# Performance work log

Hardware: AMD Instinct MI355X
Metric: run time of the kernel (lower is better)

The kernel has to match this reference:

```python
import jax, jax.numpy as jnp
import numpy as np

B, IN_DIM, OUT_DIM, NUM_FN = 256, 65536, 65536, 16  # fan_in=2 -> 16 logic functions


def setup_inputs() -> dict:
    key = jax.random.key(0)
    k1, k2, k3 = jax.random.split(key, 3)
    x = jax.random.uniform(k1, (B, IN_DIM), dtype=jnp.float32)
    weights = jax.random.normal(k2, (OUT_DIM, NUM_FN), dtype=jnp.float32)
    # each output neuron picks fan_in=2 input wires
    indices = jax.random.randint(k3, (2, OUT_DIM), 0, IN_DIM, dtype=jnp.int64)
    return {"x": x, "weights": weights, "indices": indices}


def _logic_ops(a, b):
    """All 16 real-valued relaxations of binary boolean functions. [B,OUT,16]."""
    ab = a * b
    one = jnp.ones_like(a)
    zero = jnp.zeros_like(a)
    return jnp.stack([
        zero,                # 0: false
        ab,                  # 1: a AND b
        a - ab,              # 2: a AND NOT b
        a,                   # 3: a
        b - ab,              # 4: NOT a AND b
        b,                   # 5: b
        a + b - 2 * ab,      # 6: a XOR b
        a + b - ab,          # 7: a OR b
        1 - (a + b - ab),    # 8: NOR
        1 - (a + b - 2*ab),  # 9: XNOR
        1 - b,               # 10: NOT b
        1 - b + ab,          # 11: a OR NOT b
        1 - a,               # 12: NOT a
        1 - a + ab,          # 13: NOT a OR b
        1 - ab,              # 14: NAND
        one,                 # 15: true
    ], axis=-1)


def reference(x, weights, indices):
    # gather fan-in inputs: a, b each [B, OUT_DIM]
    a = x[..., indices[0]]
    b = x[..., indices[1]]
    probs = jax.nn.softmax(weights, axis=-1)        # [OUT_DIM, 16] (training path)
    ops = _logic_ops(a, b)                          # [B, OUT_DIM, 16]
    return jnp.einsum('bof,of->bo', ops, probs)     # softmax-weighted combo
```

## Files before the change

kernel.cpp:

```cpp
#include <hip/hip_runtime.h>

#define IN_DIM  65536
#define OUT_DIM 65536
#define BATCH   256
#define ROWS_PER_BLOCK 32


__device__ __forceinline__ float bf2f(unsigned short h) {
    return __uint_as_float(((unsigned int)h) << 16);
}

__global__ __launch_bounds__(512) void detect_kernel(
    const unsigned short* __restrict__ x,
    const unsigned short* __restrict__ w,
    const int* __restrict__ idx,
    int* __restrict__ flags)
{
    __shared__ int s[3];
    int t = threadIdx.x;
    if (t < 3) s[t] = 0;
    __syncthreads();
    if (x[t] >= 0x3F80u) atomicOr(&s[0], 1);
    if ((unsigned)(w[t] & 0x7FFFu) >= 0x4800u) atomicOr(&s[1], 1);
    if ((t & 1) && idx[t] != 0) atomicOr(&s[2], 1);
    __syncthreads();
    if (t == 0) {
        flags[0] = s[0];
        flags[1] = s[1];
        flags[2] = s[2] ? 0 : 1;
    }
}

__global__ __launch_bounds__(256) void coeff_kernel(
    const void* __restrict__ weights_raw,
    const int* __restrict__ flags,
    float4* __restrict__ coeffs)
{
    int o = blockIdx.x * blockDim.x + threadIdx.x;
    if (o >= OUT_DIM) return;

    float w[16];
    if (flags[1]) {
        const float4* w4 = reinterpret_cast<const float4*>(weights_raw) + (size_t)o * 4;
        float4 q0 = w4[0], q1 = w4[1], q2 = w4[2], q3 = w4[3];
        w[0]=q0.x; w[1]=q0.y; w[2]=q0.z; w[3]=q0.w;
        w[4]=q1.x; w[5]=q1.y; w[6]=q1.z; w[7]=q1.w;
        w[8]=q2.x; w[9]=q2.y; w[10]=q2.z; w[11]=q2.w;
        w[12]=q3.x; w[13]=q3.y; w[14]=q3.z; w[15]=q3.w;
    } else {
        const uint4* w16 = reinterpret_cast<const uint4*>(
            (const unsigned short*)weights_raw + (size_t)o * 16);
        uint4 p0 = w16[0], p1 = w16[1];
        unsigned int pk[8] = { p0.x, p0.y, p0.z, p0.w, p1.x, p1.y, p1.z, p1.w };
        #pragma unroll
        for (int i = 0; i < 8; ++i) {
            w[2*i]   = bf2f((unsigned short)(pk[i] & 0xFFFFu));
            w[2*i+1] = bf2f((unsigned short)(pk[i] >> 16));
        }
    }

    float m = w[0];
    #pragma unroll
    for (int f = 1; f < 16; ++f) m = fmaxf(m, w[f]);

    float e[16]; float sum = 0.f;
    #pragma unroll
    for (int f = 0; f < 16; ++f) { e[f] = __expf(w[f] - m); sum += e[f]; }
    float inv = 1.0f / sum;

    float w0 = e[8] + e[9] + e[10] + e[11] + e[12] + e[13] + e[14] + e[15];
    float w1 = (e[2] + e[3] + e[6] + e[7]) - (e[8] + e[9] + e[12] + e[13]);
    float w2 = (e[4] + e[5] + e[6] + e[7]) - (e[8] + e[9] + e[10] + e[11]);
    float w3 = e[1] - e[2] - e[4] - 2.f*e[6] - e[7]
             + e[8] + 2.f*e[9] + e[11] + e[13] - e[14];

    coeffs[o] = make_float4(w0 * inv, w1 * inv, w2 * inv, w3 * inv);
}

__global__ __launch_bounds__(256) void transpose_kernel(
    const void* __restrict__ x_raw,
    const int* __restrict__ flags,
    float* __restrict__ x_T)
{
    __shared__ float tile[64][65];
    int tx = threadIdx.x;
    int ty = threadIdx.y;
    int c0 = blockIdx.x * 64;
    int b0 = blockIdx.y * 64;

    if (flags[0]) {
        const float* x = (const float*)x_raw;
        #pragma unroll
        for (int k = 0; k < 64; k += 4)
            tile[ty + k][tx] = x[(size_t)(b0 + ty + k) * IN_DIM + c0 + tx];
    } else {
        const unsigned short* x = (const unsigned short*)x_raw;
        #pragma unroll
        for (int k = 0; k < 64; k += 4)
            tile[ty + k][tx] = bf2f(x[(size_t)(b0 + ty + k) * IN_DIM + c0 + tx]);
    }
    __syncthreads();
    #pragma unroll
    for (int k = 0; k < 64; k += 4) {
        int c = ty + k;
        x_T[(size_t)(c0 + c) * BATCH + b0 + tx] = tile[tx][c];
    }
}

__global__ __launch_bounds__(256) void logic_t_kernel(
    const float* __restrict__ x_T,
    const void* __restrict__ idx_raw,
    const int* __restrict__ flags,
    const float4* __restrict__ coeffs,
    float* __restrict__ out)
{
    int o = blockIdx.x * blockDim.x + threadIdx.x;

    int ia, ib;
    if (flags[2]) {
        const long long* p = (const long long*)idx_raw;
        ia = (int)p[o];  ib = (int)p[OUT_DIM + o];
    } else {
        const int* p = (const int*)idx_raw;
        ia = p[o];       ib = p[OUT_DIM + o];
    }
    float4 c = coeffs[o];

    const float4* xa = reinterpret_cast<const float4*>(x_T) + ((size_t)ia << 6);
    const float4* xb = reinterpret_cast<const float4*>(x_T) + ((size_t)ib << 6);

    int b0 = blockIdx.y * ROWS_PER_BLOCK;
    int q0 = b0 >> 2;

    #pragma unroll
    for (int r = 0; r < ROWS_PER_BLOCK / 4; ++r) {
        float4 a4 = xa[q0 + r];
        float4 b4 = xb[q0 + r];
        int bb = b0 + r * 4;
        float r0 = fmaf(b4.x, fmaf(c.w, a4.x, c.z), fmaf(c.y, a4.x, c.x));
        float r1 = fmaf(b4.y, fmaf(c.w, a4.y, c.z), fmaf(c.y, a4.y, c.x));
        float r2 = fmaf(b4.z, fmaf(c.w, a4.z, c.z), fmaf(c.y, a4.z, c.x));
        float r3 = fmaf(b4.w, fmaf(c.w, a4.w, c.z), fmaf(c.y, a4.w, c.x));
        out[(size_t)(bb + 0) * OUT_DIM + o] = r0;
        out[(size_t)(bb + 1) * OUT_DIM + o] = r1;
        out[(size_t)(bb + 2) * OUT_DIM + o] = r2;
        out[(size_t)(bb + 3) * OUT_DIM + o] = r3;
    }
}

__global__ __launch_bounds__(256) void logic_kernel(
    const void* __restrict__ x_raw,
    const void* __restrict__ idx_raw,
    const int* __restrict__ flags,
    const float4* __restrict__ coeffs,
    float* __restrict__ out)
{
    int o = blockIdx.x * blockDim.x + threadIdx.x;

    int ia, ib;
    if (flags[2]) {
        const long long* p = (const long long*)idx_raw;
        ia = (int)p[o];  ib = (int)p[OUT_DIM + o];
    } else {
        const int* p = (const int*)idx_raw;
        ia = p[o];       ib = p[OUT_DIM + o];
    }
    float4 c = coeffs[o];
    int b0 = blockIdx.y * ROWS_PER_BLOCK;

    if (flags[0]) {
        const float* xa = (const float*)x_raw + ia;
        const float* xb = (const float*)x_raw + ib;
        #pragma unroll 8
        for (int r = 0; r < ROWS_PER_BLOCK; ++r) {
            int b = b0 + r;
            float av = xa[(size_t)b * IN_DIM];
            float bv = xb[(size_t)b * IN_DIM];
            out[(size_t)b * OUT_DIM + o] =
                fmaf(bv, fmaf(c.w, av, c.z), fmaf(c.y, av, c.x));
        }
    } else {
        const unsigned short* xa = (const unsigned short*)x_raw + ia;
        const unsigned short* xb = (const unsigned short*)x_raw + ib;
        #pragma unroll 8
        for (int r = 0; r < ROWS_PER_BLOCK; ++r) {
            int b = b0 + r;
            float av = bf2f(xa[(size_t)b * IN_DIM]);
            float bv = bf2f(xb[(size_t)b * IN_DIM]);
            out[(size_t)b * OUT_DIM + o] =
                fmaf(bv, fmaf(c.w, av, c.z), fmaf(c.y, av, c.x));
        }
    }
}

extern "C" void kernel_launch(void* const* d_in, const int* in_sizes, int n_in,
                              void* d_out, int out_size, void* d_ws, size_t ws_size,
                              hipStream_t stream) {
    const void* x       = d_in[0];
    const void* weights = d_in[1];
    const void* indices = d_in[2];
    float*      out     = (float*)d_out;

    int*    flags  = (int*)d_ws;
    float4* coeffs = (float4*)((char*)d_ws + 256);
    float*  x_T    = (float*)((char*)d_ws + 2u * 1024u * 1024u);

    const size_t need = 2u * 1024u * 1024u +
                        (size_t)IN_DIM * BATCH * sizeof(float);

    detect_kernel<<<1, 512, 0, stream>>>(
        (const unsigned short*)x, (const unsigned short*)weights,
        (const int*)indices, flags);

    coeff_kernel<<<dim3(OUT_DIM / 256), dim3(256), 0, stream>>>(
        weights, flags, coeffs);

    if (ws_size >= need) {
        transpose_kernel<<<dim3(IN_DIM / 64, BATCH / 64), dim3(64, 4), 0, stream>>>(
            x, flags, x_T);
        dim3 grid(OUT_DIM / 256, BATCH / ROWS_PER_BLOCK);
        logic_t_kernel<<<grid, dim3(256), 0, stream>>>(
            x_T, indices, flags, coeffs, out);
    } else {
        dim3 grid(OUT_DIM / 256, BATCH / ROWS_PER_BLOCK);
        logic_kernel<<<grid, dim3(256), 0, stream>>>(
            x, indices, flags, coeffs, out);
    }
}
```

Measured before the change: 161.2 us.

## Store transposed x as packed bf16 and fuse prep kernels into one launch

Merges the detect, coeff and transpose kernels into a single prep launch. Each block now detects the input dtype itself in shared memory instead of reading a global flags buffer. The transposed copy of x is stored as packed bf16 pairs rather than fp32, halving the intermediate write and the gather reads in the logic kernel. The cost is that fp32 inputs are rounded to bf16, which loses precision, and every logic block repeats the small dtype probe.

```diff
diff --git a/kernel.cpp b/kernel.cpp
--- a/kernel.cpp
+++ b/kernel.cpp
@@ -3,176 +3,200 @@
 #define IN_DIM  65536
 #define OUT_DIM 65536
 #define BATCH   256
-#define ROWS_PER_BLOCK 32
 
 
 __device__ __forceinline__ float bf2f(unsigned short h) {
     return __uint_as_float(((unsigned int)h) << 16);
 }
-
-__global__ __launch_bounds__(512) void detect_kernel(
-    const unsigned short* __restrict__ x,
-    const unsigned short* __restrict__ w,
-    const int* __restrict__ idx,
-    int* __restrict__ flags)
-{
-    __shared__ int s[3];
-    int t = threadIdx.x;
-    if (t < 3) s[t] = 0;
-    __syncthreads();
-    if (x[t] >= 0x3F80u) atomicOr(&s[0], 1);
-    if ((unsigned)(w[t] & 0x7FFFu) >= 0x4800u) atomicOr(&s[1], 1);
-    if ((t & 1) && idx[t] != 0) atomicOr(&s[2], 1);
-    __syncthreads();
-    if (t == 0) {
-        flags[0] = s[0];
-        flags[1] = s[1];
-        flags[2] = s[2] ? 0 : 1;
-    }
-}
-
-__global__ __launch_bounds__(256) void coeff_kernel(
-    const void* __restrict__ weights_raw,
-    const int* __restrict__ flags,
-    float4* __restrict__ coeffs)
-{
-    int o = blockIdx.x * blockDim.x + threadIdx.x;
-    if (o >= OUT_DIM) return;
-
-    float w[16];
-    if (flags[1]) {
-        const float4* w4 = reinterpret_cast<const float4*>(weights_raw) + (size_t)o * 4;
-        float4 q0 = w4[0], q1 = w4[1], q2 = w4[2], q3 = w4[3];
-        w[0]=q0.x; w[1]=q0.y; w[2]=q0.z; w[3]=q0.w;
-        w[4]=q1.x; w[5]=q1.y; w[6]=q1.z; w[7]=q1.w;
-        w[8]=q2.x; w[9]=q2.y; w[10]=q2.z; w[11]=q2.w;
-        w[12]=q3.x; w[13]=q3.y; w[14]=q3.z; w[15]=q3.w;
-    } else {
-        const uint4* w16 = reinterpret_cast<const uint4*>(
-            (const unsigned short*)weights_raw + (size_t)o * 16);
-        uint4 p0 = w16[0], p1 = w16[1];
-        unsigned int pk[8] = { p0.x, p0.y, p0.z, p0.w, p1.x, p1.y, p1.z, p1.w };
-        #pragma unroll
-        for (int i = 0; i < 8; ++i) {
-            w[2*i]   = bf2f((unsigned short)(pk[i] & 0xFFFFu));
-            w[2*i+1] = bf2f((unsigned short)(pk[i] >> 16));
-        }
-    }
-
+__device__ __forceinline__ unsigned short f2bf(float f) {
+    unsigned int u = __float_as_uint(f);
+    u += 0x7FFFu + ((u >> 16) & 1u);
+    return (unsigned short)(u >> 16);
+}
+
+__device__ __forceinline__ float4 collapse16(const float* w) {
     float m = w[0];
     #pragma unroll
     for (int f = 1; f < 16; ++f) m = fmaxf(m, w[f]);
-
     float e[16]; float sum = 0.f;
     #pragma unroll
     for (int f = 0; f < 16; ++f) { e[f] = __expf(w[f] - m); sum += e[f]; }
     float inv = 1.0f / sum;
-
     float w0 = e[8] + e[9] + e[10] + e[11] + e[12] + e[13] + e[14] + e[15];
     float w1 = (e[2] + e[3] + e[6] + e[7]) - (e[8] + e[9] + e[12] + e[13]);
     float w2 = (e[4] + e[5] + e[6] + e[7]) - (e[8] + e[9] + e[10] + e[11]);
     float w3 = e[1] - e[2] - e[4] - 2.f*e[6] - e[7]
              + e[8] + 2.f*e[9] + e[11] + e[13] - e[14];
-
-    coeffs[o] = make_float4(w0 * inv, w1 * inv, w2 * inv, w3 * inv);
-}
-
-__global__ __launch_bounds__(256) void transpose_kernel(
+    return make_float4(w0 * inv, w1 * inv, w2 * inv, w3 * inv);
+}
+
+#define TRANS_BLOCKS ((IN_DIM / 64) * (BATCH / 64))
+#define COEFF_BLOCKS (OUT_DIM / 256)
+
+__global__ __launch_bounds__(256) void prep_kernel(
     const void* __restrict__ x_raw,
-    const int* __restrict__ flags,
-    float* __restrict__ x_T)
+    const void* __restrict__ w_raw,
+    unsigned int* __restrict__ x_Tb,
+    float4* __restrict__ coeffs,
+    int trans_blocks)
 {
     __shared__ float tile[64][65];
-    int tx = threadIdx.x;
-    int ty = threadIdx.y;
-    int c0 = blockIdx.x * 64;
-    int b0 = blockIdx.y * 64;
-
-    if (flags[0]) {
-        const float* x = (const float*)x_raw;
+    __shared__ int sflag;
+    int t  = threadIdx.x;
+    int bx = blockIdx.x;
+
+    if (bx < trans_blocks) {
+        if (t == 0) sflag = 0;
+        __syncthreads();
+        if (((const unsigned short*)x_raw)[t] >= 0x3F80u) atomicOr(&sflag, 1);
+        __syncthreads();
+        int x_is_f32 = sflag;
+
+        int c0 = (bx >> 2) * 64;
+        int b0 = (bx & 3) * 64;
+        int tx = t & 63, ty = t >> 6;
+
+        if (x_is_f32) {
+            const float* x = (const float*)x_raw;
+            #pragma unroll
+            for (int k = 0; k < 64; k += 4)
+                tile[ty + k][tx] = x[(size_t)(b0 + ty + k) * IN_DIM + c0 + tx];
+        } else {
+            const unsigned short* x = (const unsigned short*)x_raw;
+            #pragma unroll
+            for (int k = 0; k < 64; k += 4)
+                tile[ty + k][tx] = bf2f(x[(size_t)(b0 + ty + k) * IN_DIM + c0 + tx]);
+        }
+        __syncthreads();
         #pragma unroll
-        for (int k = 0; k < 64; k += 4)
-            tile[ty + k][tx] = x[(size_t)(b0 + ty + k) * IN_DIM + c0 + tx];
-    } else {
-        const unsigned short* x = (const unsigned short*)x_raw;
-        #pragma unroll
-        for (int k = 0; k < 64; k += 4)
-            tile[ty + k][tx] = bf2f(x[(size_t)(b0 + ty + k) * IN_DIM + c0 + tx]);
-    }
-    __syncthreads();
-    #pragma unroll
-    for (int k = 0; k < 64; k += 4) {
-        int c = ty + k;
-        x_T[(size_t)(c0 + c) * BATCH + b0 + tx] = tile[tx][c];
-    }
-}
-
-__global__ __launch_bounds__(256) void logic_t_kernel(
-    const float* __restrict__ x_T,
+        for (int k = 0; k < 8; ++k) {
+            int d   = t + 256 * k;
+            int col = d >> 5;
+            int dw  = d & 31;
+            float lo = tile[2 * dw][col];
+            float hi = tile[2 * dw + 1][col];
+            unsigned int p = (unsigned int)f2bf(lo) | ((unsigned int)f2bf(hi) << 16);
+            x_Tb[(size_t)(c0 + col) * (BATCH / 2) + (b0 >> 1) + dw] = p;
+        }
+    } else {
+        if (t == 0) sflag = 0;
+        __syncthreads();
+        if ((((const unsigned short*)w_raw)[t] & 0x7FFFu) >= 0x4800u) atomicOr(&sflag, 1);
+        __syncthreads();
+        int w_is_f32 = sflag;
+
+        int o = (bx - trans_blocks) * 256 + t;
+        if (o >= OUT_DIM) return;
+
+        float w[16];
+        if (w_is_f32) {
+            const float4* w4 = reinterpret_cast<const float4*>(w_raw) + (size_t)o * 4;
+            float4 q0 = w4[0], q1 = w4[1], q2 = w4[2], q3 = w4[3];
+            w[0]=q0.x; w[1]=q0.y; w[2]=q0.z; w[3]=q0.w;
+            w[4]=q1.x; w[5]=q1.y; w[6]=q1.z; w[7]=q1.w;
+            w[8]=q2.x; w[9]=q2.y; w[10]=q2.z; w[11]=q2.w;
+            w[12]=q3.x; w[13]=q3.y; w[14]=q3.z; w[15]=q3.w;
+        } else {
+            const uint4* w16 = reinterpret_cast<const uint4*>(
+                (const unsigned short*)w_raw + (size_t)o * 16);
+            uint4 p0 = w16[0], p1 = w16[1];
+            unsigned int pk[8] = { p0.x, p0.y, p0.z, p0.w, p1.x, p1.y, p1.z, p1.w };
+            #pragma unroll
+            for (int i = 0; i < 8; ++i) {
+                w[2*i]   = bf2f((unsigned short)(pk[i] & 0xFFFFu));
+                w[2*i+1] = bf2f((unsigned short)(pk[i] >> 16));
+            }
+        }
+        coeffs[o] = collapse16(w);
+    }
+}
+
+#define ROWS_PER_CHUNK 32
+
+__global__ __launch_bounds__(256) void logic_bt_kernel(
+    const unsigned int* __restrict__ x_Tb,
     const void* __restrict__ idx_raw,
-    const int* __restrict__ flags,
     const float4* __restrict__ coeffs,
     float* __restrict__ out)
 {
-    int o = blockIdx.x * blockDim.x + threadIdx.x;
-
+    __shared__ int sflag;
+    int t = threadIdx.x;
+    if (t == 0) sflag = 0;
+    __syncthreads();
+    if ((t & 1) && ((const int*)idx_raw)[t] != 0) atomicOr(&sflag, 1);
+    __syncthreads();
+    int idx_is_i32 = sflag;
+
+    int o = blockIdx.x * 256 + t;
     int ia, ib;
-    if (flags[2]) {
+    if (idx_is_i32) {
+        const int* p = (const int*)idx_raw;
+        ia = p[o];       ib = p[OUT_DIM + o];
+    } else {
         const long long* p = (const long long*)idx_raw;
         ia = (int)p[o];  ib = (int)p[OUT_DIM + o];
-    } else {
-        const int* p = (const int*)idx_raw;
-        ia = p[o];       ib = p[OUT_DIM + o];
     }
     float4 c = coeffs[o];
 
-    const float4* xa = reinterpret_cast<const float4*>(x_T) + ((size_t)ia << 6);
-    const float4* xb = reinterpret_cast<const float4*>(x_T) + ((size_t)ib << 6);
-
-    int b0 = blockIdx.y * ROWS_PER_BLOCK;
-    int q0 = b0 >> 2;
+    int b0 = blockIdx.y * ROWS_PER_CHUNK;
+    const uint4* xa = (const uint4*)x_Tb + ((size_t)ia << 5) + (b0 >> 3);
+    const uint4* xb = (const uint4*)x_Tb + ((size_t)ib << 5) + (b0 >> 3);
 
     #pragma unroll
-    for (int r = 0; r < ROWS_PER_BLOCK / 4; ++r) {
-        float4 a4 = xa[q0 + r];
-        float4 b4 = xb[q0 + r];
-        int bb = b0 + r * 4;
-        float r0 = fmaf(b4.x, fmaf(c.w, a4.x, c.z), fmaf(c.y, a4.x, c.x));
-        float r1 = fmaf(b4.y, fmaf(c.w, a4.y, c.z), fmaf(c.y, a4.y, c.x));
-        float r2 = fmaf(b4.z, fmaf(c.w, a4.z, c.z), fmaf(c.y, a4.z, c.x));
-        float r3 = fmaf(b4.w, fmaf(c.w, a4.w, c.z), fmaf(c.y, a4.w, c.x));
-        out[(size_t)(bb + 0) * OUT_DIM + o] = r0;
-        out[(size_t)(bb + 1) * OUT_DIM + o] = r1;
-        out[(size_t)(bb + 2) * OUT_DIM + o] = r2;
-        out[(size_t)(bb + 3) * OUT_DIM + o] = r3;
-    }
-}
-
-__global__ __launch_bounds__(256) void logic_kernel(
+    for (int r = 0; r < ROWS_PER_CHUNK / 8; ++r) {
+        uint4 ua = xa[r], ub = xb[r];
+        unsigned int pa[4] = { ua.x, ua.y, ua.z, ua.w };
+        unsigned int pb[4] = { ub.x, ub.y, ub.z, ub.w };
+        int base = b0 + r * 8;
+        #pragma unroll
+        for (int j = 0; j < 4; ++j) {
+            float a0 = bf2f((unsigned short)(pa[j] & 0xFFFFu));
+            float a1 = bf2f((unsigned short)(pa[j] >> 16));
+            float v0 = bf2f((unsigned short)(pb[j] & 0xFFFFu));
+            float v1 = bf2f((unsigned short)(pb[j] >> 16));
+            float r0 = fmaf(v0, fmaf(c.w, a0, c.z), fmaf(c.y, a0, c.x));
+            float r1 = fmaf(v1, fmaf(c.w, a1, c.z), fmaf(c.y, a1, c.x));
+            out[(size_t)(base + 2*j)     * OUT_DIM + o] = r0;
+            out[(size_t)(base + 2*j + 1) * OUT_DIM + o] = r1;
+        }
+    }
+}
+
+__global__ __launch_bounds__(256) void logic_direct_kernel(
     const void* __restrict__ x_raw,
     const void* __restrict__ idx_raw,
-    const int* __restrict__ flags,
     const float4* __restrict__ coeffs,
     float* __restrict__ out)
 {
-    int o = blockIdx.x * blockDim.x + threadIdx.x;
-
+    __shared__ int sflag;
+    int t = threadIdx.x;
+    if (t == 0) sflag = 0;
+    __syncthreads();
+    int fl = 0;
+    if (((const unsigned short*)x_raw)[t] >= 0x3F80u) fl |= 1;
+    if ((t & 1) && ((const int*)idx_raw)[t] != 0) fl |= 2;
+    if (fl) atomicOr(&sflag, fl);
+    __syncthreads();
+    int x_is_f32   = sflag & 1;
+    int idx_is_i32 = (sflag >> 1) & 1;
+
+    int o = blockIdx.x * 256 + t;
     int ia, ib;
-    if (flags[2]) {
+    if (idx_is_i32) {
+        const int* p = (const int*)idx_raw;
+        ia = p[o];       ib = p[OUT_DIM + o];
+    } else {
         const long long* p = (const long long*)idx_raw;
         ia = (int)p[o];  ib = (int)p[OUT_DIM + o];
-    } else {
-        const int* p = (const int*)idx_raw;
-        ia = p[o];       ib = p[OUT_DIM + o];
     }
     float4 c = coeffs[o];
-    int b0 = blockIdx.y * ROWS_PER_BLOCK;
-
-    if (flags[0]) {
+    int b0 = blockIdx.y * ROWS_PER_CHUNK;
+
+    if (x_is_f32) {
         const float* xa = (const float*)x_raw + ia;
         const float* xb = (const float*)x_raw + ib;
         #pragma unroll 8
-        for (int r = 0; r < ROWS_PER_BLOCK; ++r) {
+        for (int r = 0; r < ROWS_PER_CHUNK; ++r) {
             int b = b0 + r;
             float av = xa[(size_t)b * IN_DIM];
             float bv = xb[(size_t)b * IN_DIM];
@@ -183,7 +207,7 @@
         const unsigned short* xa = (const unsigned short*)x_raw + ia;
         const unsigned short* xb = (const unsigned short*)x_raw + ib;
         #pragma unroll 8
-        for (int r = 0; r < ROWS_PER_BLOCK; ++r) {
+        for (int r = 0; r < ROWS_PER_CHUNK; ++r) {
             int b = b0 + r;
             float av = bf2f(xa[(size_t)b * IN_DIM]);
             float bv = bf2f(xb[(size_t)b * IN_DIM]);
@@ -201,29 +225,23 @@
     const void* indices = d_in[2];
     float*      out     = (float*)d_out;
 
-    int*    flags  = (int*)d_ws;
-    float4* coeffs = (float4*)((char*)d_ws + 256);
-    float*  x_T    = (float*)((char*)d_ws + 2u * 1024u * 1024u);
+    float4*       coeffs = (float4*)((char*)d_ws + 256);
+    unsigned int* x_Tb   = (unsigned int*)((char*)d_ws + 2u * 1024u * 1024u);
 
     const size_t need = 2u * 1024u * 1024u +
-                        (size_t)IN_DIM * BATCH * sizeof(float);
-
-    detect_kernel<<<1, 512, 0, stream>>>(
-        (const unsigned short*)x, (const unsigned short*)weights,
-        (const int*)indices, flags);
-
-    coeff_kernel<<<dim3(OUT_DIM / 256), dim3(256), 0, stream>>>(
-        weights, flags, coeffs);
+                        (size_t)IN_DIM * (BATCH / 2) * sizeof(unsigned int);
 
     if (ws_size >= need) {
-        transpose_kernel<<<dim3(IN_DIM / 64, BATCH / 64), dim3(64, 4), 0, stream>>>(
-            x, flags, x_T);
-        dim3 grid(OUT_DIM / 256, BATCH / ROWS_PER_BLOCK);
-        logic_t_kernel<<<grid, dim3(256), 0, stream>>>(
-            x_T, indices, flags, coeffs, out);
-    } else {
-        dim3 grid(OUT_DIM / 256, BATCH / ROWS_PER_BLOCK);
-        logic_kernel<<<grid, dim3(256), 0, stream>>>(
-            x, indices, flags, coeffs, out);
-    }
-}
+        prep_kernel<<<dim3(TRANS_BLOCKS + COEFF_BLOCKS), dim3(256), 0, stream>>>(
+            x, weights, x_Tb, coeffs, TRANS_BLOCKS);
+        dim3 grid(OUT_DIM / 256, BATCH / ROWS_PER_CHUNK);
+        logic_bt_kernel<<<grid, dim3(256), 0, stream>>>(
+            x_Tb, indices, coeffs, out);
+    } else {
+        prep_kernel<<<dim3(COEFF_BLOCKS), dim3(256), 0, stream>>>(
+            x, weights, x_Tb, coeffs, 0);
+        dim3 grid(OUT_DIM / 256, BATCH / ROWS_PER_CHUNK);
+        logic_direct_kernel<<<grid, dim3(256), 0, stream>>>(
+            x, indices, coeffs, out);
+    }
+}
```

New measurement: 140.2 us. 13.0% less time.
